# Optimization experiments

Hardware: AMD Instinct MI355X
Metric: run time of the kernel (lower is better)

## Reference

```python
import jax, jax.numpy as jnp
import numpy as np

S, B, I, H, NH, HD, ML = 512, 32, 768, 256, 8, 32, 512
LN_EPS = 1e-5


def setup_inputs() -> dict:
    key = jax.random.key(0)
    ks = jax.random.split(key, 12)
    r = lambda k, shp, s=0.05: jax.random.normal(k, shp, dtype=jnp.float32) * s
    return {
        'x': r(ks[0], (S, B, I), 1.0),
        'Wi': r(ks[1], (5 * H, I)), 'bi': jnp.zeros((5 * H,), jnp.float32),
        'Wh': r(ks[2], (5 * H, H)), 'bh': jnp.zeros((5 * H,), jnp.float32),
        'Wt': r(ks[3], (H, 3 * H)), 'bt': jnp.zeros((H,), jnp.float32),
        'Wq': r(ks[4], (3, H, H)), 'bq': jnp.zeros((3, H), jnp.float32),
        'Wk': r(ks[5], (3, H, H)), 'bk': jnp.zeros((3, H), jnp.float32),
        'Wv': r(ks[6], (3, H, H)), 'bv': jnp.zeros((3, H), jnp.float32),
        'Wo': r(ks[7], (3, H, H)), 'bo': jnp.zeros((3, H), jnp.float32),
        'relpos': r(ks[8], (3, NH, ML, HD), 1.0),
        'ln_g': jnp.ones((H,), jnp.float32), 'ln_b': jnp.zeros((H,), jnp.float32),
    }


def cumsoftmax(z):
    return jnp.cumsum(jax.nn.softmax(z, axis=-1), axis=-1)


def _forward(x, Wi, bi, Wh, bh, Wt, bt, Wq, bq, Wk, bk, Wv, bv, Wo, bo, relpos, ln_g, ln_b):
    # --- sequential PFN (ON-LSTM style) recurrence over time ---
    def step(carry, xt):
        h, c_in = carry
        gates = xt @ Wi.T + bi + h @ Wh.T + bh            # [B, 5H]
        c, eg_cin, rg_cin, eg_c, rg_c = jnp.split(gates, 5, axis=-1)
        eg_cin = 1.0 - cumsoftmax(eg_cin)
        rg_cin = cumsoftmax(rg_cin)
        eg_c = 1.0 - cumsoftmax(eg_c)
        rg_c = cumsoftmax(rg_c)
        c = jnp.tanh(c)
        ov_c = rg_c * eg_c
        up_c = rg_c - ov_c
        dn_c = eg_c - ov_c
        ov_i = rg_cin * eg_cin
        up_i = rg_cin - ov_i
        dn_i = eg_cin - ov_i
        share = ov_i * c_in + ov_c * c
        c_re = up_i * c_in + up_c * c + share
        c_ner = dn_i * c_in + dn_c * c + share
        h_re = jnp.tanh(c_re)
        h_ner = jnp.tanh(c_ner)
        h_share = jnp.tanh(share)
        c_out = jnp.concatenate([c_re, c_ner, share], axis=-1) @ Wt.T + bt
        h_out = jnp.tanh(c_out)
        return (h_out, c_out), (h_ner, h_re, h_share)

    init = (jnp.zeros((B, H), x.dtype), jnp.zeros((B, H), x.dtype))
    _, (h_ner, h_re, h_share) = jax.lax.scan(step, init, x)   # each [S, B, H]

    # --- relative multi-head attention (no 1/sqrt(d) scaling, as in source) ---
    def attn(hb, i):
        b, s, d = hb.shape
        q = (hb @ Wq[i].T + bq[i]).reshape(b, s, NH, HD)
        k = (hb @ Wk[i].T + bk[i]).reshape(b, s, NH, HD)
        v = (hb @ Wv[i].T + bv[i]).reshape(b, s, NH, HD)
        scores = jnp.einsum('bqnd,bknd->bnqk', q, k) \
               + jnp.einsum('bqnd,nkd->bnqk', q, relpos[i][:, :s])
        w = jax.nn.softmax(scores, axis=-1)
        o = jnp.einsum('bnqk,bknd->bqnd', w, v).reshape(b, s, d)
        return o @ Wo[i].T + bo[i]

    def layer_norm(z):
        m = z.mean(-1, keepdims=True)
        v = z.var(-1, keepdims=True)
        return (z - m) / jnp.sqrt(v + LN_EPS) * ln_g + ln_b

    def apply_attention(h_sbd, i):
        hb = jnp.transpose(h_sbd, (1, 0, 2))      # [B, S, H]
        y = layer_norm(hb + attn(hb, i))          # residual + LN (dropout=0, eval)
        return jnp.transpose(y, (1, 0, 2))        # back to [S, B, H]

    out_ner = apply_attention(h_ner, 0)
    out_re = apply_attention(h_re, 1)
    out_share = apply_attention(h_re, 2)  # faithful to source: h_share attn consumes h_re
    return out_ner, out_re, out_share


def reference(x, Wi, bi, Wh, bh, Wt, bt, Wq, bq, Wk, bk, Wv, bv, Wo, bo, relpos, ln_g, ln_b):
    return _forward(x, Wi, bi, Wh, bh, Wt, bt, Wq, bq, Wk, bk, Wv, bv, Wo, bo, relpos, ln_g, ln_b)
```

## Files before the change

### kernel.cpp

```cpp
#include <hip/hip_runtime.h>
#include <hip/hip_bf16.h>

#define SDIM 512
#define BDIM 32

typedef _Float16 v2h __attribute__((ext_vector_type(2)));
typedef short bf16x8 __attribute__((ext_vector_type(8)));
typedef float f32x4 __attribute__((ext_vector_type(4)));

__device__ __forceinline__ float b2f(ushort u) {
    union { uint32_t i; float f; } v; v.i = ((uint32_t)u) << 16; return v.f;
}
__device__ __forceinline__ ushort f2b(float f) {
    union { float f; uint32_t i; } v; v.f = f;
    uint32_t u = v.i;
    return (ushort)((u + 0x7fffu + ((u >> 16) & 1u)) >> 16);
}
__device__ __forceinline__ ushort f2h(float f) {
    union { _Float16 h; ushort u; } v; v.h = (_Float16)f; return v.u;
}
__device__ __forceinline__ float dot2(uint32_t w, uint32_t h, float acc) {
#if __has_builtin(__builtin_amdgcn_fdot2)
    union { uint32_t u; v2h v; } a, b;
    a.u = w; b.u = h;
    return __builtin_amdgcn_fdot2(a.v, b.v, acc, false);
#else
    union { uint32_t u; v2h v; } a, b;
    a.u = w; b.u = h;
    return acc + (float)a.v.x * (float)b.v.x + (float)a.v.y * (float)b.v.y;
#endif
}
__device__ __forceinline__ float ftanh(float x) {
    const float t = __expf(2.f * x);
    return 1.f - 2.f * __builtin_amdgcn_rcpf(t + 1.f);
}

#define DCHUNK8C(WQ, HQ, ACC)                                                  \
    {                                                                          \
        uint4 wA = *(const uint4*)(WQ);                                        \
        uint4 wB = *(const uint4*)((WQ) + 4);                                  \
        uint4 hA = *(const uint4*)(HQ);                                        \
        uint4 hB = *(const uint4*)((HQ) + 4);                                  \
        ACC = dot2(wA.x, hA.x, ACC);                                           \
        ACC = dot2(wA.y, hA.y, ACC);                                           \
        ACC = dot2(wA.z, hA.z, ACC);                                           \
        ACC = dot2(wA.w, hA.w, ACC);                                           \
        ACC = dot2(wB.x, hB.x, ACC);                                           \
        ACC = dot2(wB.y, hB.y, ACC);                                           \
        ACC = dot2(wB.z, hB.z, ACC);                                           \
        ACC = dot2(wB.w, hB.w, ACC);                                           \
    }

__global__ __launch_bounds__(256) void transpose_kernel(
    const float* __restrict__ src, float* __restrict__ dst, int R, int C)
{
    __shared__ float t[32][33];
    const int bx = blockIdx.x * 32, by = blockIdx.y * 32;
    const int x = threadIdx.x & 31, y = threadIdx.x >> 5;
    #pragma unroll
    for (int dy = 0; dy < 32; dy += 8)
        t[y + dy][x] = src[(size_t)(by + y + dy) * C + bx + x];
    __syncthreads();
    #pragma unroll
    for (int dy = 0; dy < 32; dy += 8)
        dst[(size_t)(bx + y + dy) * R + by + x] = t[x][y + dy];
}

__global__ __launch_bounds__(256) void pack8_kernel(
    const float* __restrict__ in, uint32_t* __restrict__ out, int P, int J)
{
    const int idx = blockIdx.x * 256 + threadIdx.x;
    if (idx >= P * J) return;
    const int p = idx / J, j = idx - p * J;
    const ushort lo = f2h(in[(size_t)(2 * p) * J + j]);
    const ushort hi = f2h(in[(size_t)(2 * p + 1) * J + j]);
    out[(((size_t)(p >> 3) * J + j) << 3) + (p & 7)] = ((uint32_t)hi << 16) | lo;
}

__global__ __launch_bounds__(256) void cvt_bf16_kernel(
    const float* __restrict__ in, ushort* __restrict__ out, int n)
{
    const int stride = gridDim.x * 256;
    for (int i = blockIdx.x * 256 + threadIdx.x; i < n; i += stride)
        out[i] = f2b(in[i]);
}

__global__ __launch_bounds__(256) void addvec_kernel(
    const float* __restrict__ a, const float* __restrict__ b,
    float* __restrict__ o, int n)
{
    const int i = blockIdx.x * 256 + threadIdx.x;
    if (i < n) o[i] = a[i] + b[i];
}

template<bool ASWAP, bool RELPOS>
__global__ __launch_bounds__(256) void mfma_gemm_kernel(
    const ushort* __restrict__ A16, const ushort* __restrict__ B16,
    const float* __restrict__ bias, const float* __restrict__ rp,
    float* __restrict__ C, int M, int N, int K)
{
    __shared__ ushort As[64][40];
    __shared__ ushort Bs[64][40];
    const int tid = threadIdx.x;
    const int tile_m = blockIdx.x * 64, tile_n = blockIdx.y * 64;
    const int r = tid >> 2, c = (tid & 3) * 8;
    const int am = tile_m + r;
    const int ar = ASWAP ? ((am & (SDIM - 1)) * BDIM + (am >> 9)) : am;
    const int bn = tile_n + r;
    const int w = tid >> 6, lane = tid & 63;
    const int mi = lane & 15, quad = lane >> 4;
    f32x4 acc[4] = {};

    for (int k0 = 0; k0 < K; k0 += 32) {
        *(uint4*)&As[r][c] = *(const uint4*)(A16 + (size_t)ar * K + k0 + c);
        *(uint4*)&Bs[r][c] = *(const uint4*)(B16 + (size_t)bn * K + k0 + c);
        __syncthreads();
        const bf16x8 af = *(const bf16x8*)&As[w * 16 + mi][quad * 8];
        #pragma unroll
        for (int j = 0; j < 4; j++) {
            const bf16x8 bf = *(const bf16x8*)&Bs[j * 16 + mi][quad * 8];
            acc[j] = __builtin_amdgcn_mfma_f32_16x16x32_bf16(af, bf, acc[j], 0, 0, 0);
        }
        __syncthreads();
    }
    #pragma unroll
    for (int j = 0; j < 4; j++) {
        const int gn = tile_n + j * 16 + mi;
        const float bv = bias[gn];
        #pragma unroll
        for (int rr = 0; rr < 4; rr++) {
            const int gm = tile_m + w * 16 + quad * 4 + rr;
            float v = acc[j][rr] + bv;
            if (RELPOS) {
                const int sgm = gm & (SDIM - 1);
                v += rp[((gn >> 5) << 14) + (sgm << 5) + (gn & 31)];
            }
            C[(size_t)gm * N + gn] = v;
        }
    }
}

__global__ __launch_bounds__(1024) void scan_kernel(
    const float* __restrict__ gx,
    const uint32_t* __restrict__ Wh8,
    const uint32_t* __restrict__ Wt8,
    const float* __restrict__ bt,
    ushort* __restrict__ h_ner,
    ushort* __restrict__ h_re)
{
    const int b = blockIdx.x;
    const int tid = threadIdx.x;
    __shared__ float cs[256], g[1280], ext[1024];
    __shared__ alignas(16) uint32_t hs_pk[128];
    __shared__ alignas(16) uint32_t cat_pk[384];
    __shared__ float rsum[16];
    if (tid < 256) cs[tid] = 0.f;
    if (tid < 128) hs_pk[tid] = 0u;
    __syncthreads();
    const int lane = tid & 63;
    const int ch = tid >> 8;
    const int wch = (tid >> 6) & 3;
    const int er = tid & 255;
    const int ep = tid >> 8;
    const uint32_t* wmain = Wh8 + (size_t)tid * 8;
    const uint32_t* wext  = Wh8 + ((size_t)(ep * 4) * 1280 + 1024 + er) * 8;
    const uint32_t* wtp   = Wt8 + ((size_t)(ep * 12) * 256 + er) * 8;

    for (int t = 0; t < SDIM; t++) {
        const float* gxr = gx + (size_t)(t * BDIM + b) * 1280;
        {
            float a0 = 0.f, a1 = 0.f;
            #pragma unroll 2
            for (int q8 = 0; q8 < 16; q8 += 2) {
                DCHUNK8C(wmain + (size_t)q8 * (1280 * 8), hs_pk + q8 * 8, a0);
                DCHUNK8C(wmain + (size_t)(q8 + 1) * (1280 * 8), hs_pk + q8 * 8 + 8, a1);
            }
            g[tid] = gxr[tid] + a0 + a1;
        }
        {
            float ae = (ep == 0) ? gxr[1024 + er] : 0.f;
            #pragma unroll
            for (int i = 0; i < 4; i++)
                DCHUNK8C(wext + (size_t)i * (1280 * 8), hs_pk + (ep * 4 + i) * 8, ae);
            ext[ep * 256 + er] = ae;
        }
        __syncthreads();
        if (tid < 256) g[tid] = ftanh(g[tid]);
        float v;
        if (tid >= 768) {
            const int r_ = tid - 768;
            v = ext[r_] + ext[256 + r_] + ext[512 + r_] + ext[768 + r_];
        } else {
            v = g[256 + tid];
        }
        const float e = __expf(v);
        float wsum = e;
        #pragma unroll
        for (int off = 32; off >= 1; off >>= 1) wsum += __shfl_xor(wsum, off, 64);
        if (lane == 0) rsum[ch * 4 + wch] = wsum;
        float cum = e;
        #pragma unroll
        for (int off = 1; off <= 32; off <<= 1) {
            float tsh = __shfl_up(cum, (unsigned)off, 64);
            if (lane >= off) cum += tsh;
        }
        __syncthreads();
        const float tot = rsum[ch * 4] + rsum[ch * 4 + 1] + rsum[ch * 4 + 2] + rsum[ch * 4 + 3];
        float prev = 0.f;
        if (wch > 0) prev += rsum[ch * 4];
        if (wch > 1) prev += rsum[ch * 4 + 1];
        if (wch > 2) prev += rsum[ch * 4 + 2];
        float r = (cum + prev) * __builtin_amdgcn_rcpf(tot);
        if (ch == 0 || ch == 2) r = 1.f - r;
        g[256 + tid] = r;
        __syncthreads();
        if (tid < 256) {
            const float c = g[tid];
            const float egi = g[256 + tid], rgi = g[512 + tid];
            const float egc = g[768 + tid], rgc = g[1024 + tid];
            const float cin = cs[tid];
            const float ovc = rgc * egc, upc = rgc - ovc, dnc = egc - ovc;
            const float ovi = rgi * egi, upi = rgi - ovi, dni = egi - ovi;
            const float share = ovi * cin + ovc * c;
            const float cre = upi * cin + upc * c + share;
            const float cner = dni * cin + dnc * c + share;
            ((_Float16*)cat_pk)[tid]       = (_Float16)cre;
            ((_Float16*)cat_pk)[256 + tid] = (_Float16)cner;
            ((_Float16*)cat_pk)[512 + tid] = (_Float16)share;
            const size_t ob = (size_t)(t * BDIM + b) * 256 + tid;
            h_re[ob] = f2b(ftanh(cre));
            h_ner[ob] = f2b(ftanh(cner));
        }
        __syncthreads();
        {
            float s0 = 0.f, s1 = 0.f;
            #pragma unroll 2
            for (int i = 0; i < 12; i += 2) {
                DCHUNK8C(wtp + (size_t)i * (256 * 8), cat_pk + (ep * 12 + i) * 8, s0);
                DCHUNK8C(wtp + (size_t)(i + 1) * (256 * 8), cat_pk + (ep * 12 + i + 1) * 8, s1);
            }
            g[ep * 256 + er] = s0 + s1;
        }
        __syncthreads();
        if (tid < 256) {
            const float co = g[tid] + g[256 + tid] + g[512 + tid] + g[768 + tid] + bt[tid];
            cs[tid] = co;
            ((_Float16*)hs_pk)[tid] = (_Float16)ftanh(co);
        }
        __syncthreads();
    }
}

__global__ __launch_bounds__(512) void attn_kernel(
    const float* __restrict__ q_ws, const float* __restrict__ kk_ws,
    const float* __restrict__ v_ws, ushort* __restrict__ o16)
{
    __shared__ float sc[8 * 516];
    __shared__ float ps[8 * 256];
    __shared__ float sinv[8];
    const int bn = blockIdx.x;
    const int b = bn >> 3, n = bn & 7;
    const int tid = threadIdx.x;
    const int w = tid >> 6, lane = tid & 63;
    const int ki = w * 64 + lane;
    float kv[32];
    {
        const float4* kp = (const float4*)(kk_ws + (size_t)(b * 512 + ki) * 256 + n * 32);
        #pragma unroll
        for (int d4 = 0; d4 < 8; d4++) {
            float4 x = kp[d4];
            kv[4 * d4] = x.x; kv[4 * d4 + 1] = x.y; kv[4 * d4 + 2] = x.z; kv[4 * d4 + 3] = x.w;
        }
    }
    const int rr = lane >> 3, dq = lane & 7;

    for (int q0 = 0; q0 < 512; q0 += 8) {
        const float* qbase = q_ws + (size_t)(b * 512 + q0) * 256 + n * 32;
        #pragma unroll 1
        for (int r = 0; r < 8; r++) {
            const float* qr = qbase + r * 256;
            float s = 0.f;
            #pragma unroll
            for (int d = 0; d < 32; d++) s += qr[d] * kv[d];
            sc[r * 516 + ki] = s;
        }
        __syncthreads();
        {
            float* row = sc + w * 516;
            float4 a = ((const float4*)row)[lane];
            float4 c4 = ((const float4*)row)[lane + 64];
            float mx = fmaxf(fmaxf(fmaxf(a.x, a.y), fmaxf(a.z, a.w)),
                             fmaxf(fmaxf(c4.x, c4.y), fmaxf(c4.z, c4.w)));
            #pragma unroll
            for (int off = 32; off >= 1; off >>= 1) mx = fmaxf(mx, __shfl_xor(mx, off, 64));
            a.x = __expf(a.x - mx); a.y = __expf(a.y - mx);
            a.z = __expf(a.z - mx); a.w = __expf(a.w - mx);
            c4.x = __expf(c4.x - mx); c4.y = __expf(c4.y - mx);
            c4.z = __expf(c4.z - mx); c4.w = __expf(c4.w - mx);
            float sm = a.x + a.y + a.z + a.w + c4.x + c4.y + c4.z + c4.w;
            #pragma unroll
            for (int off = 32; off >= 1; off >>= 1) sm += __shfl_xor(sm, off, 64);
            ((float4*)row)[lane] = a;
            ((float4*)row)[lane + 64] = c4;
            if (lane == 0) sinv[w] = 1.f / sm;
        }
        __syncthreads();
        {
            float4 acc = {0.f, 0.f, 0.f, 0.f};
            const float* erow = sc + rr * 516 + w * 64;
            const float* vbase = v_ws + (size_t)(b * 512 + w * 64) * 256 + n * 32 + dq * 4;
            #pragma unroll 8
            for (int j = 0; j < 64; j++) {
                const float e = erow[j];
                float4 vv = *(const float4*)(vbase + (size_t)j * 256);
                acc.x += e * vv.x; acc.y += e * vv.y; acc.z += e * vv.z; acc.w += e * vv.w;
            }
            ((float4*)ps)[tid] = acc;
        }
        __syncthreads();
        if (tid < 256) {
            const int r2 = tid >> 5, d = tid & 31;
            float s = 0.f;
            #pragma unroll
            for (int ww = 0; ww < 8; ww++) s += ps[ww * 256 + r2 * 32 + d];
            o16[(size_t)(b * 512 + q0 + r2) * 256 + n * 32 + d] = f2b(s * sinv[r2]);
        }
        __syncthreads();
    }
}

__global__ __launch_bounds__(256) void ln_kernel(
    const float* __restrict__ proj, const ushort* __restrict__ hsrc,
    const float* __restrict__ lng, const float* __restrict__ lnb,
    float* __restrict__ outp)
{
    const int m = blockIdx.x;
    const int j = threadIdx.x;
    const int b = m >> 9, s = m & 511;
    const size_t oidx = (size_t)(s * 32 + b) * 256 + j;
    const float y = proj[(size_t)m * 256 + j] + b2f(hsrc[oidx]);
    float sum = y, sq = y * y;
    #pragma unroll
    for (int off = 32; off >= 1; off >>= 1) {
        sum += __shfl_xor(sum, off, 64);
        sq += __shfl_xor(sq, off, 64);
    }
    __shared__ float r1[4], r2[4];
    const int wv = j >> 6;
    if ((j & 63) == 0) { r1[wv] = sum; r2[wv] = sq; }
    __syncthreads();
    const float ts = r1[0] + r1[1] + r1[2] + r1[3];
    const float tq = r2[0] + r2[1] + r2[2] + r2[3];
    const float mean = ts * (1.f / 256.f);
    const float var = tq * (1.f / 256.f) - mean * mean;
    const float o = (y - mean) * rsqrtf(var + 1e-5f) * lng[j] + lnb[j];
    outp[oidx] = o;
}

extern "C" void kernel_launch(void* const* d_in, const int* in_sizes, int n_in,
                              void* d_out, int out_size, void* d_ws, size_t ws_size,
                              hipStream_t stream) {
    (void)in_sizes; (void)n_in; (void)out_size; (void)ws_size;
    const float* x   = (const float*)d_in[0];
    const float* Wi  = (const float*)d_in[1];
    const float* bi  = (const float*)d_in[2];
    const float* Wh  = (const float*)d_in[3];
    const float* bh  = (const float*)d_in[4];
    const float* Wt  = (const float*)d_in[5];
    const float* bt  = (const float*)d_in[6];
    const float* Wq  = (const float*)d_in[7];
    const float* bq  = (const float*)d_in[8];
    const float* Wk  = (const float*)d_in[9];
    const float* bk  = (const float*)d_in[10];
    const float* Wv  = (const float*)d_in[11];
    const float* bv  = (const float*)d_in[12];
    const float* Wo  = (const float*)d_in[13];
    const float* bo  = (const float*)d_in[14];
    const float* rp  = (const float*)d_in[15];
    const float* lng = (const float*)d_in[16];
    const float* lnb = (const float*)d_in[17];
    float* outp = (float*)d_out;

    float* ws = (float*)d_ws;
    float* gx    = ws;
    float* q_ws  = ws;
    float* kk_ws = ws + 4194304;
    float* v_ws  = ws + 8388608;
    float* pj_ws = ws + 12582912;
    ushort* o16  = (ushort*)(ws + 16777216);
    ushort* hner16 = (ushort*)(ws + 20971520);
    ushort* hre16  = (ushort*)(ws + 23068672);
    uint32_t* Wh8 = (uint32_t*)(ws + 25165824);
    uint32_t* Wt8 = (uint32_t*)(ws + 25329664);
    ushort* Wq16 = (ushort*)(ws + 25427968);
    ushort* Wk16 = (ushort*)(ws + 25526272);
    ushort* Wv16 = (ushort*)(ws + 25624576);
    ushort* Wo16 = (ushort*)(ws + 25722880);

    ushort* x16  = (ushort*)outp;
    ushort* Wi16 = (ushort*)(outp + 6291456);
    float* WhT   = outp + 6782976;
    float* WtT   = outp + 7110656;
    float* bsum  = outp + 7307264;

    transpose_kernel<<<dim3(8, 40), 256, 0, stream>>>(Wh, WhT, 1280, 256);
    transpose_kernel<<<dim3(24, 8), 256, 0, stream>>>(Wt, WtT, 256, 768);
    pack8_kernel<<<dim3(640), 256, 0, stream>>>(WhT, Wh8, 128, 1280);
    pack8_kernel<<<dim3(384), 256, 0, stream>>>(WtT, Wt8, 384, 256);
    addvec_kernel<<<dim3(5), 256, 0, stream>>>(bi, bh, bsum, 1280);
    cvt_bf16_kernel<<<dim3(4096), 256, 0, stream>>>(x, x16, 12582912);
    cvt_bf16_kernel<<<dim3(1024), 256, 0, stream>>>(Wi, Wi16, 983040);
    cvt_bf16_kernel<<<dim3(256), 256, 0, stream>>>(Wq, Wq16, 196608);
    cvt_bf16_kernel<<<dim3(256), 256, 0, stream>>>(Wk, Wk16, 196608);
    cvt_bf16_kernel<<<dim3(256), 256, 0, stream>>>(Wv, Wv16, 196608);
    cvt_bf16_kernel<<<dim3(256), 256, 0, stream>>>(Wo, Wo16, 196608);

    mfma_gemm_kernel<false, false><<<dim3(256, 20), 256, 0, stream>>>(
        x16, Wi16, bsum, nullptr, gx, 16384, 1280, 768);

    scan_kernel<<<dim3(32), dim3(1024), 0, stream>>>(gx, Wh8, Wt8, bt, hner16, hre16);

    for (int i = 0; i < 3; i++) {
        const ushort* src16 = (i == 0) ? hner16 : hre16;
        mfma_gemm_kernel<true, false><<<dim3(256, 4), 256, 0, stream>>>(
            src16, Wq16 + (size_t)i * 65536, bq + i * 256, nullptr, q_ws, 16384, 256, 256);
        mfma_gemm_kernel<true, true><<<dim3(256, 4), 256, 0, stream>>>(
            src16, Wk16 + (size_t)i * 65536, bk + i * 256, rp + (size_t)i * 131072, kk_ws, 16384, 256, 256);
        mfma_gemm_kernel<true, false><<<dim3(256, 4), 256, 0, stream>>>(
            src16, Wv16 + (size_t)i * 65536, bv + i * 256, nullptr, v_ws, 16384, 256, 256);
        attn_kernel<<<dim3(256), dim3(512), 0, stream>>>(q_ws, kk_ws, v_ws, o16);
        mfma_gemm_kernel<false, false><<<dim3(256, 4), 256, 0, stream>>>(
            o16, Wo16 + (size_t)i * 65536, bo + i * 256, nullptr, pj_ws, 16384, 256, 256);
        ln_kernel<<<dim3(16384), dim3(256), 0, stream>>>(
            pj_ws, src16, lng, lnb, outp + (size_t)i * 4194304);
    }
}
```

Baseline: 6.408 ms.

## Split scan recurrence across four cooperating blocks per batch with flag sync

The sequential scan is split from one block per batch element into four blocks, each computing a quarter of the K-dimension of the Wh and Wt matvecs. Partial sums go to global memory, and per-step progress flags are exchanged through spin-waits with agent-scope atomics, twice per timestep. This spreads the per-step weight reads and FMA work over four times as many CUs to shorten the serial critical path. The cost is two global round-trips and inter-block barriers every step. It also assumes all 128 blocks are co-resident, and otherwise relies on a spin timeout.

```diff
diff --git a/kernel.cpp b/kernel.cpp
--- a/kernel.cpp
+++ b/kernel.cpp
@@ -51,6 +51,9 @@
         ACC = dot2(wB.w, hB.w, ACC);                                           \
     }
 
+#define ALOAD(P) __hip_atomic_load((P), __ATOMIC_RELAXED, __HIP_MEMORY_SCOPE_AGENT)
+#define ASTORE(P, V) __hip_atomic_store((P), (V), __ATOMIC_RELAXED, __HIP_MEMORY_SCOPE_AGENT)
+
 __global__ __launch_bounds__(256) void transpose_kernel(
     const float* __restrict__ src, float* __restrict__ dst, int R, int C)
 {
@@ -91,6 +94,12 @@
 {
     const int i = blockIdx.x * 256 + threadIdx.x;
     if (i < n) o[i] = a[i] + b[i];
+}
+
+__global__ __launch_bounds__(256) void zero_kernel(int* __restrict__ p, int n)
+{
+    const int i = blockIdx.x * 256 + threadIdx.x;
+    if (i < n) p[i] = 0;
 }
 
 template<bool ASWAP, bool RELPOS>
@@ -146,11 +155,16 @@
     const uint32_t* __restrict__ Wt8,
     const float* __restrict__ bt,
     ushort* __restrict__ h_ner,
-    ushort* __restrict__ h_re)
-{
-    const int b = blockIdx.x;
+    ushort* __restrict__ h_re,
+    float* __restrict__ Pg,
+    float* __restrict__ PC,
+    int* __restrict__ FA,
+    int* __restrict__ FC)
+{
+    const int bs = blockIdx.x;
+    const int b = bs & 31, s = bs >> 5;
     const int tid = threadIdx.x;
-    __shared__ float cs[256], g[1280], ext[1024];
+    __shared__ float cs[256], g[1280];
     __shared__ alignas(16) uint32_t hs_pk[128];
     __shared__ alignas(16) uint32_t cat_pk[384];
     __shared__ float rsum[16];
@@ -162,37 +176,55 @@
     const int wch = (tid >> 6) & 3;
     const int er = tid & 255;
     const int ep = tid >> 8;
-    const uint32_t* wmain = Wh8 + (size_t)tid * 8;
-    const uint32_t* wext  = Wh8 + ((size_t)(ep * 4) * 1280 + 1024 + er) * 8;
-    const uint32_t* wtp   = Wt8 + ((size_t)(ep * 12) * 256 + er) * 8;
+    const uint32_t* wA0 = Wh8 + ((size_t)(4 * s) * 1280 + tid) * 8;
+    const uint32_t* wA1 = Wh8 + ((size_t)(4 * s) * 1280 + 1024 + tid) * 8;
+    const uint32_t* wC = Wt8 + ((size_t)(12 * s + 3 * ep) * 256 + er) * 8;
+    float* myPg = Pg + (size_t)bs * 1280;
+    float* myPC = PC + (size_t)bs * 256;
+    const float* Pgb = Pg + (size_t)b * 1280;
+    const float* PCb = PC + (size_t)b * 256;
 
     for (int t = 0; t < SDIM; t++) {
         const float* gxr = gx + (size_t)(t * BDIM + b) * 1280;
+        float a0 = 0.f, a1 = 0.f, ax0 = 0.f, ax1 = 0.f;
         {
-            float a0 = 0.f, a1 = 0.f;
-            #pragma unroll 2
-            for (int q8 = 0; q8 < 16; q8 += 2) {
-                DCHUNK8C(wmain + (size_t)q8 * (1280 * 8), hs_pk + q8 * 8, a0);
-                DCHUNK8C(wmain + (size_t)(q8 + 1) * (1280 * 8), hs_pk + q8 * 8 + 8, a1);
+            const uint32_t* hq = hs_pk + 32 * s;
+            DCHUNK8C(wA0 + (size_t)0 * 10240, hq + 0, a0);
+            DCHUNK8C(wA0 + (size_t)1 * 10240, hq + 8, a1);
+            DCHUNK8C(wA0 + (size_t)2 * 10240, hq + 16, a0);
+            DCHUNK8C(wA0 + (size_t)3 * 10240, hq + 24, a1);
+            if (tid < 256) {
+                DCHUNK8C(wA1 + (size_t)0 * 10240, hq + 0, ax0);
+                DCHUNK8C(wA1 + (size_t)1 * 10240, hq + 8, ax1);
+                DCHUNK8C(wA1 + (size_t)2 * 10240, hq + 16, ax0);
+                DCHUNK8C(wA1 + (size_t)3 * 10240, hq + 24, ax1);
             }
-            g[tid] = gxr[tid] + a0 + a1;
-        }
+        }
+        ASTORE(myPg + tid, a0 + a1);
+        if (tid < 256) ASTORE(myPg + 1024 + tid, ax0 + ax1);
+        __syncthreads();
+        if (tid == 0) ASTORE(FA + bs * 16, t + 1);
+        if (tid < 3) {
+            const int sp = (s + 1 + tid) & 3;
+            const int* fp = FA + (sp * 32 + b) * 16;
+            int spins = 0;
+            while (ALOAD(fp) < t + 1 && ++spins < (1 << 26))
+                __builtin_amdgcn_s_sleep(1);
+        }
+        __syncthreads();
         {
-            float ae = (ep == 0) ? gxr[1024 + er] : 0.f;
-            #pragma unroll
-            for (int i = 0; i < 4; i++)
-                DCHUNK8C(wext + (size_t)i * (1280 * 8), hs_pk + (ep * 4 + i) * 8, ae);
-            ext[ep * 256 + er] = ae;
+            float v = gxr[tid] + ALOAD(Pgb + tid) + ALOAD(Pgb + 40960 + tid)
+                    + ALOAD(Pgb + 81920 + tid) + ALOAD(Pgb + 122880 + tid);
+            g[tid] = v;
+            if (tid < 256) {
+                const int rr_ = 1024 + tid;
+                g[rr_] = gxr[rr_] + ALOAD(Pgb + rr_) + ALOAD(Pgb + 40960 + rr_)
+                       + ALOAD(Pgb + 81920 + rr_) + ALOAD(Pgb + 122880 + rr_);
+            }
         }
         __syncthreads();
         if (tid < 256) g[tid] = ftanh(g[tid]);
-        float v;
-        if (tid >= 768) {
-            const int r_ = tid - 768;
-            v = ext[r_] + ext[256 + r_] + ext[512 + r_] + ext[768 + r_];
-        } else {
-            v = g[256 + tid];
-        }
+        const float v = g[256 + tid];
         const float e = __expf(v);
         float wsum = e;
         #pragma unroll
@@ -227,23 +259,39 @@
             ((_Float16*)cat_pk)[tid]       = (_Float16)cre;
             ((_Float16*)cat_pk)[256 + tid] = (_Float16)cner;
             ((_Float16*)cat_pk)[512 + tid] = (_Float16)share;
-            const size_t ob = (size_t)(t * BDIM + b) * 256 + tid;
-            h_re[ob] = f2b(ftanh(cre));
-            h_ner[ob] = f2b(ftanh(cner));
+            if (s == 0) {
+                const size_t ob = (size_t)(t * BDIM + b) * 256 + tid;
+                h_re[ob] = f2b(ftanh(cre));
+                h_ner[ob] = f2b(ftanh(cner));
+            }
         }
         __syncthreads();
         {
-            float s0 = 0.f, s1 = 0.f;
-            #pragma unroll 2
-            for (int i = 0; i < 12; i += 2) {
-                DCHUNK8C(wtp + (size_t)i * (256 * 8), cat_pk + (ep * 12 + i) * 8, s0);
-                DCHUNK8C(wtp + (size_t)(i + 1) * (256 * 8), cat_pk + (ep * 12 + i + 1) * 8, s1);
-            }
-            g[ep * 256 + er] = s0 + s1;
+            float s0 = 0.f, s1 = 0.f, s2 = 0.f;
+            const int pl = 12 * s + 3 * ep;
+            DCHUNK8C(wC + (size_t)0 * 2048, cat_pk + (pl + 0) * 8, s0);
+            DCHUNK8C(wC + (size_t)1 * 2048, cat_pk + (pl + 1) * 8, s1);
+            DCHUNK8C(wC + (size_t)2 * 2048, cat_pk + (pl + 2) * 8, s2);
+            g[ep * 256 + er] = s0 + s1 + s2;
         }
         __syncthreads();
         if (tid < 256) {
-            const float co = g[tid] + g[256 + tid] + g[512 + tid] + g[768 + tid] + bt[tid];
+            const float pco = g[tid] + g[256 + tid] + g[512 + tid] + g[768 + tid];
+            ASTORE(myPC + tid, pco);
+        }
+        __syncthreads();
+        if (tid == 0) ASTORE(FC + bs * 16, t + 1);
+        if (tid < 3) {
+            const int sp = (s + 1 + tid) & 3;
+            const int* fp = FC + (sp * 32 + b) * 16;
+            int spins = 0;
+            while (ALOAD(fp) < t + 1 && ++spins < (1 << 26))
+                __builtin_amdgcn_s_sleep(1);
+        }
+        __syncthreads();
+        if (tid < 256) {
+            const float co = bt[tid] + ALOAD(PCb + tid) + ALOAD(PCb + 8192 + tid)
+                           + ALOAD(PCb + 16384 + tid) + ALOAD(PCb + 24576 + tid);
             cs[tid] = co;
             ((_Float16*)hs_pk)[tid] = (_Float16)ftanh(co);
         }
@@ -402,7 +450,12 @@
     float* WhT   = outp + 6782976;
     float* WtT   = outp + 7110656;
     float* bsum  = outp + 7307264;
-
+    float* Pg    = outp + 7340032;
+    float* PC    = outp + 7503872;
+    int*   FA    = (int*)(outp + 7536640);
+    int*   FC    = (int*)(outp + 7538688);
+
+    zero_kernel<<<dim3(16), 256, 0, stream>>>(FA, 4096);
     transpose_kernel<<<dim3(8, 40), 256, 0, stream>>>(Wh, WhT, 1280, 256);
     transpose_kernel<<<dim3(24, 8), 256, 0, stream>>>(Wt, WtT, 256, 768);
     pack8_kernel<<<dim3(640), 256, 0, stream>>>(WhT, Wh8, 128, 1280);
@@ -418,7 +471,8 @@
     mfma_gemm_kernel<false, false><<<dim3(256, 20), 256, 0, stream>>>(
         x16, Wi16, bsum, nullptr, gx, 16384, 1280, 768);
 
-    scan_kernel<<<dim3(32), dim3(1024), 0, stream>>>(gx, Wh8, Wt8, bt, hner16, hre16);
+    scan_kernel<<<dim3(128), dim3(1024), 0, stream>>>(
+        gx, Wh8, Wt8, bt, hner16, hre16, Pg, PC, FA, FC);
 
     for (int i = 0; i < 3; i++) {
         const ushort* src16 = (i == 0) ? hner16 : hre16;
```

Measured after the change: 6.822 ms. 1.06x slower.
